# Kernel tuning notes

Measured on AMD Instinct MI355X. Metric: run time of the kernel, lower is better.

The kernel has to match this reference:

```python
import jax, jax.numpy as jnp
import numpy as np


def setup_inputs() -> dict:
    key = jax.random.key(0)
    x = jax.random.normal(key, (4, 4096, 128), dtype=jnp.float32)
    return {"x": x}


def reference(x) -> jnp.ndarray:
    # Unnormalized bilinear self-attention with Q=K=V=x (no softmax).
    # scores[b,t,s] = sum_d x[b,t,d] x[b,s,d]; out[b,t,d] = sum_s scores[b,t,s] x[b,s,d]
    scores = jnp.einsum('btd,bsd->bts', x, x)  # [B,T,T]
    out = jnp.einsum('bts,bsd->btd', scores, x)  # [B,T,D]
    return out
```

## Files before the change

### kernel.cpp

```cpp
#include <hip/hip_runtime.h>

#define BATCH 4
#define T 4096
#define D 128
#define P 8
#define KROWS 512
#define ROWS 64
#define ST1 72
#define S2 136

typedef __attribute__((ext_vector_type(4))) float f32x4;
typedef __attribute__((ext_vector_type(8))) short bf16x8;

__device__ __forceinline__ unsigned short f2b(float f) {
    unsigned u = __builtin_bit_cast(unsigned, f);
    u += 0x7FFFu + ((u >> 16) & 1u);
    return (unsigned short)(u >> 16);
}

#define STAGE_CHUNK(XPBASE, DST)                                               \
    {                                                                          \
        _Pragma("unroll")                                                      \
        for (int pass = 0; pass < 8; pass++) {                                 \
            const int slot = (tid >> 6) + 4 * pass;                            \
            const int dd = 2 * (tid & 7) + 16 * (slot & 7);                    \
            const int tpg = ((tid >> 3) & 7) + 8 * (slot >> 3);                \
            const int t = 2 * tpg;                                             \
            float2 f0 = *(const float2*)((XPBASE) + (size_t)t * D + dd);       \
            float2 f1 = *(const float2*)((XPBASE) + (size_t)(t + 1) * D + dd); \
            unsigned u0 = (unsigned)f2b(f0.x) | ((unsigned)f2b(f1.x) << 16);   \
            unsigned u1 = (unsigned)f2b(f0.y) | ((unsigned)f2b(f1.y) << 16);   \
            *(unsigned*)((DST) + dd * ST1 + 2 * tpg) = u0;                     \
            *(unsigned*)((DST) + (dd + 1) * ST1 + 2 * tpg) = u1;               \
        }                                                                      \
    }

__global__ __launch_bounds__(256) void k_part(const float* __restrict__ x,
                                              unsigned short* __restrict__ part) {
    __shared__ unsigned short XT[2 * D * ST1];
    const int blk = blockIdx.x;
    const int b = blk >> 3, p = blk & 7;
    const float* xp = x + ((size_t)b * T + (size_t)p * KROWS) * D;
    const int tid = threadIdx.x;
    const int lane = tid & 63, w = tid >> 6;
    const int m = lane & 15, q = lane >> 4;
    const int m0 = w * 32;

    f32x4 acc[2][8];
    #pragma unroll
    for (int mi = 0; mi < 2; mi++)
        #pragma unroll
        for (int ni = 0; ni < 8; ni++) acc[mi][ni] = (f32x4){0.f, 0.f, 0.f, 0.f};

    STAGE_CHUNK(xp, XT);
    __syncthreads();

    #pragma unroll 1
    for (int i = 0; i < 8; i++) {
        const unsigned short* cur = XT + (i & 1) * (D * ST1);
        unsigned short* nxt = XT + ((i + 1) & 1) * (D * ST1);
        if (i < 7) {
            const float* xn = xp + (size_t)(i + 1) * ROWS * D;
            STAGE_CHUNK(xn, nxt);
        }
        #pragma unroll
        for (int s = 0; s < 2; s++) {
            bf16x8 av[2], bv[8];
            #pragma unroll
            for (int mi = 0; mi < 2; mi++)
                av[mi] = *(const bf16x8*)(cur + (m0 + mi * 16 + m) * ST1 + q * 8 + s * 32);
            #pragma unroll
            for (int ni = 0; ni < 8; ni++)
                bv[ni] = *(const bf16x8*)(cur + (ni * 16 + m) * ST1 + q * 8 + s * 32);
            #pragma unroll
            for (int mi = 0; mi < 2; mi++)
                #pragma unroll
                for (int ni = 0; ni < 8; ni++)
                    acc[mi][ni] = __builtin_amdgcn_mfma_f32_16x16x32_bf16(av[mi], bv[ni], acc[mi][ni], 0, 0, 0);
        }
        __syncthreads();
    }

    unsigned short* pp = part + (size_t)blk * (D * D);
    #pragma unroll
    for (int mi = 0; mi < 2; mi++)
        #pragma unroll
        for (int ni = 0; ni < 8; ni++) {
            const int row0 = m0 + mi * 16 + q * 4;
            const int col = ni * 16 + m;
            #pragma unroll
            for (int r = 0; r < 4; r++)
                pp[(size_t)(row0 + r) * D + col] = f2b(acc[mi][ni][r]);
        }
}

__global__ __launch_bounds__(256) void k_xg2(const float* __restrict__ x,
                                             const unsigned short* __restrict__ part,
                                             float* __restrict__ out) {
    __shared__ unsigned short Xs[ROWS * S2];
    __shared__ unsigned short Gs[D * S2];
    const int blk = blockIdx.x;
    const int b = (blk & 7) >> 1;
    const int chunk = ((blk & 1) << 5) | (blk >> 3);
    const float* xp = x + ((size_t)b * T + (size_t)chunk * ROWS) * D;
    const int tid = threadIdx.x;

    {
        const int dg = tid & 31, tr = tid >> 5;
        #pragma unroll
        for (int ii = 0; ii < 8; ii++) {
            const int t = tr + ii * 8;
            float4 v = ((const float4*)(xp + (size_t)t * D))[dg];
            ushort4 pk;
            pk.x = f2b(v.x); pk.y = f2b(v.y); pk.z = f2b(v.z); pk.w = f2b(v.w);
            *(ushort4*)(Xs + t * S2 + dg * 4) = pk;
        }
    }
    {
        const unsigned short* pb = part + (size_t)b * P * (D * D);
        #pragma unroll
        for (int i = 0; i < 8; i++) {
            const int e8 = (i * 256 + tid) * 8;
            float s[8];
            #pragma unroll
            for (int k = 0; k < 8; k++) s[k] = 0.f;
            #pragma unroll
            for (int pp = 0; pp < P; pp++) {
                uint4 v = *(const uint4*)(pb + (size_t)pp * (D * D) + e8);
                const unsigned uu[4] = {v.x, v.y, v.z, v.w};
                #pragma unroll
                for (int k = 0; k < 4; k++) {
                    s[2 * k]     += __builtin_bit_cast(float, uu[k] << 16);
                    s[2 * k + 1] += __builtin_bit_cast(float, uu[k] & 0xFFFF0000u);
                }
            }
            uint4 o;
            o.x = (unsigned)f2b(s[0]) | ((unsigned)f2b(s[1]) << 16);
            o.y = (unsigned)f2b(s[2]) | ((unsigned)f2b(s[3]) << 16);
            o.z = (unsigned)f2b(s[4]) | ((unsigned)f2b(s[5]) << 16);
            o.w = (unsigned)f2b(s[6]) | ((unsigned)f2b(s[7]) << 16);
            const int row = e8 >> 7, col = e8 & 127;
            *(uint4*)(Gs + row * S2 + col) = o;
        }
    }
    __syncthreads();

    {
        const int lane = tid & 63, w = tid >> 6;
        const int m = lane & 15, q = lane >> 4;
        f32x4 acc[8];
        #pragma unroll
        for (int ni = 0; ni < 8; ni++) acc[ni] = (f32x4){0.f, 0.f, 0.f, 0.f};

        const unsigned short* arow = Xs + (w * 16 + m) * S2 + q * 8;
        const unsigned short* brow = Gs + m * S2 + q * 8;

        #pragma unroll
        for (int s = 0; s < 4; s++) {
            bf16x8 a = *(const bf16x8*)(arow + s * 32);
            #pragma unroll
            for (int ni = 0; ni < 8; ni++) {
                bf16x8 bb = *(const bf16x8*)(brow + ni * 16 * S2 + s * 32);
                acc[ni] = __builtin_amdgcn_mfma_f32_16x16x32_bf16(a, bb, acc[ni], 0, 0, 0);
            }
        }

        float* op = out + ((size_t)b * T + (size_t)chunk * ROWS) * D;
        const int row0 = w * 16 + q * 4;
        #pragma unroll
        for (int ni = 0; ni < 8; ni++)
            #pragma unroll
            for (int r = 0; r < 4; r++)
                op[(row0 + r) * D + ni * 16 + m] = acc[ni][r];
    }
}

extern "C" void kernel_launch(void* const* d_in, const int* in_sizes, int n_in,
                              void* d_out, int out_size, void* d_ws, size_t ws_size,
                              hipStream_t stream) {
    const float* x = (const float*)d_in[0];
    float* out = (float*)d_out;

    unsigned short* part = (unsigned short*)d_ws;

    k_part<<<BATCH * P, 256, 0, stream>>>(x, part);
    k_xg2<<<BATCH * 64, 256, 0, stream>>>(x, part, out);
}
```

Baseline: 80.56 us.

## Split Gram partial computation into column strips across more blocks

The Gram partial kernel now splits the sequence into 16 chunks and the 128 output columns into 4 strips of 32, launching 256 blocks instead of 32 so the GPU's many CUs are occupied. Each block stages a 256-row slab and computes a 128x32 strip. The second kernel reduces 16 partials per strip instead of 8. The cost is redundant staging and conversion of the same x rows by four blocks, plus twice as many partials to read in the reduction.

```diff
diff --git a/kernel.cpp b/kernel.cpp
--- a/kernel.cpp
+++ b/kernel.cpp
@@ -3,8 +3,10 @@
 #define BATCH 4
 #define T 4096
 #define D 128
-#define P 8
-#define KROWS 512
+#define NP 16
+#define NS 4
+#define SW 32
+#define KR 256
 #define ROWS 64
 #define ST1 72
 #define S2 136
@@ -35,66 +37,66 @@
         }                                                                      \
     }
 
-__global__ __launch_bounds__(256) void k_part(const float* __restrict__ x,
-                                              unsigned short* __restrict__ part) {
+__global__ __launch_bounds__(256) void k_gram_strip(const float* __restrict__ x,
+                                                    unsigned short* __restrict__ part) {
     __shared__ unsigned short XT[2 * D * ST1];
     const int blk = blockIdx.x;
-    const int b = blk >> 3, p = blk & 7;
-    const float* xp = x + ((size_t)b * T + (size_t)p * KROWS) * D;
+    const int s = blk & 3, p = (blk >> 2) & 15, b = blk >> 6;
+    const float* xp = x + ((size_t)b * T + (size_t)p * KR) * D;
     const int tid = threadIdx.x;
     const int lane = tid & 63, w = tid >> 6;
     const int m = lane & 15, q = lane >> 4;
     const int m0 = w * 32;
 
-    f32x4 acc[2][8];
+    f32x4 acc[2][2];
     #pragma unroll
     for (int mi = 0; mi < 2; mi++)
         #pragma unroll
-        for (int ni = 0; ni < 8; ni++) acc[mi][ni] = (f32x4){0.f, 0.f, 0.f, 0.f};
+        for (int ni = 0; ni < 2; ni++) acc[mi][ni] = (f32x4){0.f, 0.f, 0.f, 0.f};
 
     STAGE_CHUNK(xp, XT);
     __syncthreads();
 
     #pragma unroll 1
-    for (int i = 0; i < 8; i++) {
+    for (int i = 0; i < 4; i++) {
         const unsigned short* cur = XT + (i & 1) * (D * ST1);
         unsigned short* nxt = XT + ((i + 1) & 1) * (D * ST1);
-        if (i < 7) {
+        if (i < 3) {
             const float* xn = xp + (size_t)(i + 1) * ROWS * D;
             STAGE_CHUNK(xn, nxt);
         }
         #pragma unroll
-        for (int s = 0; s < 2; s++) {
-            bf16x8 av[2], bv[8];
+        for (int ks = 0; ks < 2; ks++) {
+            bf16x8 av[2], bv[2];
             #pragma unroll
             for (int mi = 0; mi < 2; mi++)
-                av[mi] = *(const bf16x8*)(cur + (m0 + mi * 16 + m) * ST1 + q * 8 + s * 32);
+                av[mi] = *(const bf16x8*)(cur + (m0 + mi * 16 + m) * ST1 + q * 8 + ks * 32);
             #pragma unroll
-            for (int ni = 0; ni < 8; ni++)
-                bv[ni] = *(const bf16x8*)(cur + (ni * 16 + m) * ST1 + q * 8 + s * 32);
+            for (int ni = 0; ni < 2; ni++)
+                bv[ni] = *(const bf16x8*)(cur + (s * SW + ni * 16 + m) * ST1 + q * 8 + ks * 32);
             #pragma unroll
             for (int mi = 0; mi < 2; mi++)
                 #pragma unroll
-                for (int ni = 0; ni < 8; ni++)
+                for (int ni = 0; ni < 2; ni++)
                     acc[mi][ni] = __builtin_amdgcn_mfma_f32_16x16x32_bf16(av[mi], bv[ni], acc[mi][ni], 0, 0, 0);
         }
         __syncthreads();
     }
 
-    unsigned short* pp = part + (size_t)blk * (D * D);
+    unsigned short* pp = part + (size_t)blk * (D * SW);
     #pragma unroll
     for (int mi = 0; mi < 2; mi++)
         #pragma unroll
-        for (int ni = 0; ni < 8; ni++) {
+        for (int ni = 0; ni < 2; ni++) {
             const int row0 = m0 + mi * 16 + q * 4;
             const int col = ni * 16 + m;
             #pragma unroll
             for (int r = 0; r < 4; r++)
-                pp[(size_t)(row0 + r) * D + col] = f2b(acc[mi][ni][r]);
+                pp[(size_t)(row0 + r) * SW + col] = f2b(acc[mi][ni][r]);
         }
 }
 
-__global__ __launch_bounds__(256) void k_xg2(const float* __restrict__ x,
+__global__ __launch_bounds__(256) void k_xg3(const float* __restrict__ x,
                                              const unsigned short* __restrict__ part,
                                              float* __restrict__ out) {
     __shared__ unsigned short Xs[ROWS * S2];
@@ -117,30 +119,34 @@
         }
     }
     {
-        const unsigned short* pb = part + (size_t)b * P * (D * D);
-        #pragma unroll
+        #pragma unroll 2
         for (int i = 0; i < 8; i++) {
-            const int e8 = (i * 256 + tid) * 8;
-            float s[8];
+            const int g = i * 256 + tid;
+            const int s = g >> 9;
+            const int rem = g & 511;
+            const int row = rem >> 2;
+            const int c32 = (rem & 3) * 8;
+            const unsigned short* pb = part + (size_t)((b * 16) * 4 + s) * (D * SW)
+                                     + (size_t)row * SW + c32;
+            float acc8[8];
             #pragma unroll
-            for (int k = 0; k < 8; k++) s[k] = 0.f;
+            for (int k = 0; k < 8; k++) acc8[k] = 0.f;
             #pragma unroll
-            for (int pp = 0; pp < P; pp++) {
-                uint4 v = *(const uint4*)(pb + (size_t)pp * (D * D) + e8);
+            for (int p = 0; p < NP; p++) {
+                uint4 v = *(const uint4*)(pb + (size_t)p * 4 * (D * SW));
                 const unsigned uu[4] = {v.x, v.y, v.z, v.w};
                 #pragma unroll
                 for (int k = 0; k < 4; k++) {
-                    s[2 * k]     += __builtin_bit_cast(float, uu[k] << 16);
-                    s[2 * k + 1] += __builtin_bit_cast(float, uu[k] & 0xFFFF0000u);
+                    acc8[2 * k]     += __builtin_bit_cast(float, uu[k] << 16);
+                    acc8[2 * k + 1] += __builtin_bit_cast(float, uu[k] & 0xFFFF0000u);
                 }
             }
             uint4 o;
-            o.x = (unsigned)f2b(s[0]) | ((unsigned)f2b(s[1]) << 16);
-            o.y = (unsigned)f2b(s[2]) | ((unsigned)f2b(s[3]) << 16);
-            o.z = (unsigned)f2b(s[4]) | ((unsigned)f2b(s[5]) << 16);
-            o.w = (unsigned)f2b(s[6]) | ((unsigned)f2b(s[7]) << 16);
-            const int row = e8 >> 7, col = e8 & 127;
-            *(uint4*)(Gs + row * S2 + col) = o;
+            o.x = (unsigned)f2b(acc8[0]) | ((unsigned)f2b(acc8[1]) << 16);
+            o.y = (unsigned)f2b(acc8[2]) | ((unsigned)f2b(acc8[3]) << 16);
+            o.z = (unsigned)f2b(acc8[4]) | ((unsigned)f2b(acc8[5]) << 16);
+            o.w = (unsigned)f2b(acc8[6]) | ((unsigned)f2b(acc8[7]) << 16);
+            *(uint4*)(Gs + row * S2 + s * SW + c32) = o;
         }
     }
     __syncthreads();
@@ -156,11 +162,11 @@
         const unsigned short* brow = Gs + m * S2 + q * 8;
 
         #pragma unroll
-        for (int s = 0; s < 4; s++) {
-            bf16x8 a = *(const bf16x8*)(arow + s * 32);
+        for (int ks = 0; ks < 4; ks++) {
+            bf16x8 a = *(const bf16x8*)(arow + ks * 32);
             #pragma unroll
             for (int ni = 0; ni < 8; ni++) {
-                bf16x8 bb = *(const bf16x8*)(brow + ni * 16 * S2 + s * 32);
+                bf16x8 bb = *(const bf16x8*)(brow + ni * 16 * S2 + ks * 32);
                 acc[ni] = __builtin_amdgcn_mfma_f32_16x16x32_bf16(a, bb, acc[ni], 0, 0, 0);
             }
         }
@@ -183,6 +189,6 @@
 
     unsigned short* part = (unsigned short*)d_ws;
 
-    k_part<<<BATCH * P, 256, 0, stream>>>(x, part);
-    k_xg2<<<BATCH * 64, 256, 0, stream>>>(x, part, out);
+    k_gram_strip<<<BATCH * NP * NS, 256, 0, stream>>>(x, part);
+    k_xg3<<<BATCH * 64, 256, 0, stream>>>(x, part, out);
 }
```

After: 100.5 us. 1.25x slower.
